# Kernel tuning notes

Hardware: AMD Instinct MI355X
Metric: run time of the kernel (lower is better)

The kernel has to match this reference:

```python
import jax, jax.numpy as jnp
import numpy as np

HEAD_NUM = 8
QKV_DIM = 16
SQRT_EMB = 11.313708498984761  # sqrt(128)
LOGIT_CLIP = 10.0
SOFTMAX_TEMP = 0.1


def _heads(x):
    # [B, n, H*d] -> [B, H, n, d]
    b, n, _ = x.shape
    return x.reshape(b, n, HEAD_NUM, QKV_DIM).transpose(0, 2, 1, 3)


def setup_inputs() -> dict:
    key = jax.random.key(0)
    ks = jax.random.split(key, 8)
    B, P, N, E = 32, 512, 1024, 128
    s = 1.0 / np.sqrt(E)
    return {
        "encoded_last_node": jax.random.normal(ks[0], (B, P, E), jnp.float32),
        "load": jax.random.uniform(ks[1], (B, P), jnp.float32),
        "ninf_mask": jnp.zeros((B, P, N), jnp.float32),
        "encoded_nodes": jax.random.normal(ks[2], (B, N, E), jnp.float32),
        "Wq_last": jax.random.normal(ks[3], (E + 1, E), jnp.float32) * s,
        "Wk": jax.random.normal(ks[4], (E, E), jnp.float32) * s,
        "Wv": jax.random.normal(ks[5], (E, E), jnp.float32) * s,
        "Wc": jax.random.normal(ks[6], (E, E), jnp.float32) * s,
        "bc": jnp.zeros((E,), jnp.float32),
    }


def reference(encoded_last_node, load, ninf_mask, encoded_nodes, Wq_last, Wk, Wv, Wc, bc):
    # set_kv
    k = _heads(encoded_nodes @ Wk)              # [B,H,N,d]
    v = _heads(encoded_nodes @ Wv)              # [B,H,N,d]

    # forward
    input_cat = jnp.concatenate([encoded_last_node, load[:, :, None]], axis=2)  # [B,P,E+1]
    q = _heads(input_cat @ Wq_last)             # [B,H,P,d]

    score = jnp.einsum("bhpd,bhnd->bhpn", q, k) / jnp.sqrt(jnp.float32(QKV_DIM))
    score = score + ninf_mask[:, None, :, :]
    weights = jax.nn.softmax(score, axis=3)
    out = jnp.einsum("bhpn,bhnd->bhpd", weights, v)
    out_concat = out.transpose(0, 2, 1, 3).reshape(q.shape[0], q.shape[2], HEAD_NUM * QKV_DIM)
    mh_atten_out = out_concat @ Wc + bc         # [B,P,E]

    # single-head tanh-clipped scoring against encoded_nodes
    s = jnp.einsum("bpe,bne->bpn", mh_atten_out, encoded_nodes) / SQRT_EMB
    s = LOGIT_CLIP * jnp.tanh(s) + ninf_mask
    probs = jax.nn.softmax(s / SOFTMAX_TEMP, axis=2)
    return probs
```

## Files before the change

kernel.cpp:

```cpp
#include <hip/hip_runtime.h>
#include <math.h>
#include <stdint.h>

#define B_ 32
#define P_ 512
#define N_ 1024
#define E_ 128
#define H_ 8
#define D_ 16

typedef unsigned short ushort_t;
typedef __attribute__((ext_vector_type(8))) short short8;
typedef __attribute__((ext_vector_type(4))) float f32x4;

union U8 { short8 s8; uint32_t u[4]; };

__device__ __forceinline__ void fma4(float4& acc, float a, float4 w) {
  acc.x = fmaf(a, w.x, acc.x); acc.y = fmaf(a, w.y, acc.y);
  acc.z = fmaf(a, w.z, acc.z); acc.w = fmaf(a, w.w, acc.w);
}
__device__ __forceinline__ void add4(float4& acc, float4 w) {
  acc.x += w.x; acc.y += w.y; acc.z += w.z; acc.w += w.w;
}
__device__ __forceinline__ float fast_tanh(float x) {
  x = fminf(20.f, fmaxf(-20.f, x));
  float e = __expf(2.f * x);
  return (e - 1.f) / (e + 1.f);
}
__device__ __forceinline__ uint32_t f32_to_hl(float x) {
  uint32_t bits = __float_as_uint(x);
  uint32_t hi = bits >> 16;
  float rem = x - __uint_as_float(bits & 0xFFFF0000u);
  uint32_t lo = __float_as_uint(rem) >> 16;
  return hi | (lo << 16);
}

__global__ __launch_bounds__(256, 2) void gemm128(
    const float* __restrict__ A, const float* __restrict__ W,
    const float* __restrict__ ea, const float* __restrict__ ew,
    const float* __restrict__ bias, float* __restrict__ C) {
  __shared__ float As[128][33];
  __shared__ float Ws[32][128];
  const int tid = threadIdx.x;
  const size_t m0 = (size_t)blockIdx.x * 128;
  const int tr = tid >> 3, tc = tid & 7;
  const int r0 = tr * 4;
  const int c0 = tc * 16;

  float4 acc[4][4];
#pragma unroll
  for (int j = 0; j < 4; ++j)
#pragma unroll
    for (int i = 0; i < 4; ++i) acc[j][i] = make_float4(0.f, 0.f, 0.f, 0.f);

  for (int kb = 0; kb < 4; ++kb) {
    __syncthreads();
    {
      int idx = tid;
#pragma unroll
      for (int it = 0; it < 4; ++it, idx += 256) {
        int r = idx >> 3, k4 = idx & 7;
        float4 v = reinterpret_cast<const float4*>(A + (m0 + r) * 128 + kb * 32)[k4];
        As[r][k4 * 4 + 0] = v.x; As[r][k4 * 4 + 1] = v.y;
        As[r][k4 * 4 + 2] = v.z; As[r][k4 * 4 + 3] = v.w;
      }
      idx = tid;
#pragma unroll
      for (int it = 0; it < 4; ++it, idx += 256) {
        int kk = idx >> 5, c4 = idx & 31;
        reinterpret_cast<float4*>(&Ws[kk][0])[c4] =
            reinterpret_cast<const float4*>(W + (size_t)(kb * 32 + kk) * 128)[c4];
      }
    }
    __syncthreads();
#pragma unroll 8
    for (int kk = 0; kk < 32; ++kk) {
      float a0 = As[r0 + 0][kk], a1 = As[r0 + 1][kk];
      float a2 = As[r0 + 2][kk], a3 = As[r0 + 3][kk];
      const float4* wr = reinterpret_cast<const float4*>(&Ws[kk][c0]);
      float4 w0 = wr[0], w1 = wr[1], w2 = wr[2], w3 = wr[3];
      fma4(acc[0][0], a0, w0); fma4(acc[0][1], a0, w1); fma4(acc[0][2], a0, w2); fma4(acc[0][3], a0, w3);
      fma4(acc[1][0], a1, w0); fma4(acc[1][1], a1, w1); fma4(acc[1][2], a1, w2); fma4(acc[1][3], a1, w3);
      fma4(acc[2][0], a2, w0); fma4(acc[2][1], a2, w1); fma4(acc[2][2], a2, w2); fma4(acc[2][3], a2, w3);
      fma4(acc[3][0], a3, w0); fma4(acc[3][1], a3, w1); fma4(acc[3][2], a3, w2); fma4(acc[3][3], a3, w3);
    }
  }

  if (ea != nullptr) {
    const float4* ew4 = reinterpret_cast<const float4*>(ew + c0);
    float4 e0 = ew4[0], e1 = ew4[1], e2 = ew4[2], e3 = ew4[3];
#pragma unroll
    for (int j = 0; j < 4; ++j) {
      float av = ea[m0 + r0 + j];
      fma4(acc[j][0], av, e0); fma4(acc[j][1], av, e1);
      fma4(acc[j][2], av, e2); fma4(acc[j][3], av, e3);
    }
  }
  if (bias != nullptr) {
    const float4* b4 = reinterpret_cast<const float4*>(bias + c0);
    float4 b0 = b4[0], b1 = b4[1], b2 = b4[2], b3 = b4[3];
#pragma unroll
    for (int j = 0; j < 4; ++j) {
      add4(acc[j][0], b0); add4(acc[j][1], b1); add4(acc[j][2], b2); add4(acc[j][3], b3);
    }
  }
#pragma unroll
  for (int j = 0; j < 4; ++j) {
    float4* c4p = reinterpret_cast<float4*>(C + (m0 + r0 + j) * 128 + c0);
    c4p[0] = acc[j][0]; c4p[1] = acc[j][1]; c4p[2] = acc[j][2]; c4p[3] = acc[j][3];
  }
}

__global__ __launch_bounds__(256, 1) void gemm_kv(
    const float* __restrict__ A, const float* __restrict__ Wk,
    const float* __restrict__ Wv, ushort_t* __restrict__ khl,
    ushort_t* __restrict__ vthl) {
  __shared__ float As[128][33];
  __shared__ float Wks[32][128];
  __shared__ float Wvs[32][128];
  const int tid = threadIdx.x;
  const size_t m0 = (size_t)blockIdx.x * 128;
  const int tr = tid >> 3, tc = tid & 7;
  const int r0 = tr * 4;
  const int c0 = tc * 16;

  float4 acck[4][4], accv[4][4];
#pragma unroll
  for (int j = 0; j < 4; ++j)
#pragma unroll
    for (int i = 0; i < 4; ++i) {
      acck[j][i] = make_float4(0.f, 0.f, 0.f, 0.f);
      accv[j][i] = make_float4(0.f, 0.f, 0.f, 0.f);
    }

  for (int kb = 0; kb < 4; ++kb) {
    __syncthreads();
    {
      int idx = tid;
#pragma unroll
      for (int it = 0; it < 4; ++it, idx += 256) {
        int r = idx >> 3, k4 = idx & 7;
        float4 v = reinterpret_cast<const float4*>(A + (m0 + r) * 128 + kb * 32)[k4];
        As[r][k4 * 4 + 0] = v.x; As[r][k4 * 4 + 1] = v.y;
        As[r][k4 * 4 + 2] = v.z; As[r][k4 * 4 + 3] = v.w;
      }
      idx = tid;
#pragma unroll
      for (int it = 0; it < 4; ++it, idx += 256) {
        int kk = idx >> 5, c4 = idx & 31;
        reinterpret_cast<float4*>(&Wks[kk][0])[c4] =
            reinterpret_cast<const float4*>(Wk + (size_t)(kb * 32 + kk) * 128)[c4];
      }
      idx = tid;
#pragma unroll
      for (int it = 0; it < 4; ++it, idx += 256) {
        int kk = idx >> 5, c4 = idx & 31;
        reinterpret_cast<float4*>(&Wvs[kk][0])[c4] =
            reinterpret_cast<const float4*>(Wv + (size_t)(kb * 32 + kk) * 128)[c4];
      }
    }
    __syncthreads();
#pragma unroll 4
    for (int kk = 0; kk < 32; ++kk) {
      float a0 = As[r0 + 0][kk], a1 = As[r0 + 1][kk];
      float a2 = As[r0 + 2][kk], a3 = As[r0 + 3][kk];
      const float4* wkr = reinterpret_cast<const float4*>(&Wks[kk][c0]);
      const float4* wvr = reinterpret_cast<const float4*>(&Wvs[kk][c0]);
#pragma unroll
      for (int i = 0; i < 4; ++i) {
        float4 wk = wkr[i], wv = wvr[i];
        fma4(acck[0][i], a0, wk); fma4(acck[1][i], a1, wk);
        fma4(acck[2][i], a2, wk); fma4(acck[3][i], a3, wk);
        fma4(accv[0][i], a0, wv); fma4(accv[1][i], a1, wv);
        fma4(accv[2][i], a2, wv); fma4(accv[3][i], a3, wv);
      }
    }
  }

#pragma unroll
  for (int j = 0; j < 4; ++j) {
    ushort_t* krow = khl + (m0 + r0 + j) * 256;
#pragma unroll
    for (int i = 0; i < 4; ++i) {
      uint4 pk;
      pk.x = f32_to_hl(acck[j][i].x);
      pk.y = f32_to_hl(acck[j][i].y);
      pk.z = f32_to_hl(acck[j][i].z);
      pk.w = f32_to_hl(acck[j][i].w);
      *reinterpret_cast<uint4*>(krow + 2 * (c0 + 4 * i)) = pk;
    }
  }
  const int bb = (int)(m0 >> 10);
  const int nbase = (int)(m0 & 1023) + r0;
#pragma unroll
  for (int i = 0; i < 4; ++i) {
#pragma unroll
    for (int e = 0; e < 4; ++e) {
      const int c = c0 + 4 * i + e;
      const int hh = c >> 4, dd = c & 15;
      uint4 pv;
      pv.x = f32_to_hl(reinterpret_cast<const float*>(&accv[0][i])[e]);
      pv.y = f32_to_hl(reinterpret_cast<const float*>(&accv[1][i])[e]);
      pv.z = f32_to_hl(reinterpret_cast<const float*>(&accv[2][i])[e]);
      pv.w = f32_to_hl(reinterpret_cast<const float*>(&accv[3][i])[e]);
      *reinterpret_cast<uint4*>(
          vthl + (size_t)((bb * H_ + hh) * 16 + dd) * 2048 + 2 * nbase) = pv;
    }
  }
}

__global__ __launch_bounds__(256, 2) void gemm_q(
    const float* __restrict__ A, const float* __restrict__ W,
    const float* __restrict__ ea, const float* __restrict__ ew,
    ushort_t* __restrict__ qhl) {
  __shared__ float As[128][33];
  __shared__ float Ws[32][128];
  const int tid = threadIdx.x;
  const size_t m0 = (size_t)blockIdx.x * 128;
  const int tr = tid >> 3, tc = tid & 7;
  const int r0 = tr * 4;
  const int c0 = tc * 16;

  float4 acc[4][4];
#pragma unroll
  for (int j = 0; j < 4; ++j)
#pragma unroll
    for (int i = 0; i < 4; ++i) acc[j][i] = make_float4(0.f, 0.f, 0.f, 0.f);

  for (int kb = 0; kb < 4; ++kb) {
    __syncthreads();
    {
      int idx = tid;
#pragma unroll
      for (int it = 0; it < 4; ++it, idx += 256) {
        int r = idx >> 3, k4 = idx & 7;
        float4 v = reinterpret_cast<const float4*>(A + (m0 + r) * 128 + kb * 32)[k4];
        As[r][k4 * 4 + 0] = v.x; As[r][k4 * 4 + 1] = v.y;
        As[r][k4 * 4 + 2] = v.z; As[r][k4 * 4 + 3] = v.w;
      }
      idx = tid;
#pragma unroll
      for (int it = 0; it < 4; ++it, idx += 256) {
        int kk = idx >> 5, c4 = idx & 31;
        reinterpret_cast<float4*>(&Ws[kk][0])[c4] =
            reinterpret_cast<const float4*>(W + (size_t)(kb * 32 + kk) * 128)[c4];
      }
    }
    __syncthreads();
#pragma unroll 8
    for (int kk = 0; kk < 32; ++kk) {
      float a0 = As[r0 + 0][kk], a1 = As[r0 + 1][kk];
      float a2 = As[r0 + 2][kk], a3 = As[r0 + 3][kk];
      const float4* wr = reinterpret_cast<const float4*>(&Ws[kk][c0]);
      float4 w0 = wr[0], w1 = wr[1], w2 = wr[2], w3 = wr[3];
      fma4(acc[0][0], a0, w0); fma4(acc[0][1], a0, w1); fma4(acc[0][2], a0, w2); fma4(acc[0][3], a0, w3);
      fma4(acc[1][0], a1, w0); fma4(acc[1][1], a1, w1); fma4(acc[1][2], a1, w2); fma4(acc[1][3], a1, w3);
      fma4(acc[2][0], a2, w0); fma4(acc[2][1], a2, w1); fma4(acc[2][2], a2, w2); fma4(acc[2][3], a2, w3);
      fma4(acc[3][0], a3, w0); fma4(acc[3][1], a3, w1); fma4(acc[3][2], a3, w2); fma4(acc[3][3], a3, w3);
    }
  }

  {
    const float4* ew4 = reinterpret_cast<const float4*>(ew + c0);
    float4 e0 = ew4[0], e1 = ew4[1], e2 = ew4[2], e3 = ew4[3];
#pragma unroll
    for (int j = 0; j < 4; ++j) {
      float av = ea[m0 + r0 + j];
      fma4(acc[j][0], av, e0); fma4(acc[j][1], av, e1);
      fma4(acc[j][2], av, e2); fma4(acc[j][3], av, e3);
    }
  }
#pragma unroll
  for (int j = 0; j < 4; ++j) {
    ushort_t* qrow = qhl + (m0 + r0 + j) * 256;
#pragma unroll
    for (int i = 0; i < 4; ++i) {
      uint4 pq;
      pq.x = f32_to_hl(acc[j][i].x);
      pq.y = f32_to_hl(acc[j][i].y);
      pq.z = f32_to_hl(acc[j][i].z);
      pq.w = f32_to_hl(acc[j][i].w);
      *reinterpret_cast<uint4*>(qrow + 2 * (c0 + 4 * i)) = pq;
    }
  }
}

__global__ __launch_bounds__(256, 4) void attn_mfma(
    const ushort_t* __restrict__ qhl, const ushort_t* __restrict__ khl,
    const ushort_t* __restrict__ vthl, const float* __restrict__ mask,
    float* __restrict__ O) {
  const int b = blockIdx.z, h = blockIdx.y, pt = blockIdx.x;
  const int tid = threadIdx.x;
  const int w = tid >> 6, lane = tid & 63;
  const int lp = lane & 15, g = lane >> 4;
  const int pA = pt * 128 + w * 16 + lp;
  const int pB = pA + 64;

  __shared__ __align__(16) ushort_t Ks[64 * 40];
  __shared__ __align__(16) ushort_t VTs[16 * 136];

  U8 qA1u, qA2u, qB1u, qB2u;
  {
    uint4 qldA = *reinterpret_cast<const uint4*>(
        qhl + (size_t)(b * P_ + pA) * 256 + h * 32 + g * 8);
    uint4 qldB = *reinterpret_cast<const uint4*>(
        qhl + (size_t)(b * P_ + pB) * 256 + h * 32 + g * 8);
    uint32_t a[4] = {qldA.x, qldA.y, qldA.z, qldA.w};
    uint32_t c[4] = {qldB.x, qldB.y, qldB.z, qldB.w};
#pragma unroll
    for (int i = 0; i < 4; ++i) {
      uint32_t lo16 = a[i] & 0xFFFFu;
      qA1u.u[i] = lo16 | (lo16 << 16);
      qA2u.u[i] = a[i] >> 16;
      uint32_t lo16b = c[i] & 0xFFFFu;
      qB1u.u[i] = lo16b | (lo16b << 16);
      qB2u.u[i] = c[i] >> 16;
    }
  }
  const short8 qA1 = qA1u.s8, qA2 = qA2u.s8, qB1 = qB1u.s8, qB2 = qB2u.s8;

  const float* mrowA = mask + (size_t)(b * P_ + pA) * N_;
  const float* mrowB = mask + (size_t)(b * P_ + pB) * N_;

  f32x4 accA = {0.f, 0.f, 0.f, 0.f}, accB = {0.f, 0.f, 0.f, 0.f};
  float mA = -1e30f, lA = 0.f, mB = -1e30f, lB = 0.f;

  for (int ch = 0; ch < N_ / 64; ++ch) {
    const int n0 = ch * 64;
    __syncthreads();
    {
      const int n = tid >> 2, seg = tid & 3;
      uint4 kv = *reinterpret_cast<const uint4*>(
          khl + (size_t)(b * N_ + n0 + n) * 256 + h * 32 + seg * 8);
      *reinterpret_cast<uint4*>(Ks + n * 40 + seg * 8) = kv;
      const int d = tid >> 4, s2 = tid & 15;
      uint4 vv = *reinterpret_cast<const uint4*>(
          vthl + (size_t)((b * H_ + h) * 16 + d) * 2048 + n0 * 2 + s2 * 8);
      *reinterpret_cast<uint4*>(VTs + d * 136 + s2 * 8) = vv;
    }
    __syncthreads();

    float svA[4][4], svB[4][4];
    float cmA = -1e30f, cmB = -1e30f;
#pragma unroll
    for (int tt = 0; tt < 4; ++tt) {
      short8 ka = *reinterpret_cast<const short8*>(Ks + (tt * 16 + lp) * 40 + g * 8);
      f32x4 aA = {0.f, 0.f, 0.f, 0.f};
      aA = __builtin_amdgcn_mfma_f32_16x16x32_bf16(ka, qA1, aA, 0, 0, 0);
      aA = __builtin_amdgcn_mfma_f32_16x16x32_bf16(ka, qA2, aA, 0, 0, 0);
      f32x4 aB = {0.f, 0.f, 0.f, 0.f};
      aB = __builtin_amdgcn_mfma_f32_16x16x32_bf16(ka, qB1, aB, 0, 0, 0);
      aB = __builtin_amdgcn_mfma_f32_16x16x32_bf16(ka, qB2, aB, 0, 0, 0);
      float4 mvA = *reinterpret_cast<const float4*>(mrowA + n0 + tt * 16 + g * 4);
      float4 mvB = *reinterpret_cast<const float4*>(mrowB + n0 + tt * 16 + g * 4);
      svA[tt][0] = fmaf(aA[0], 0.25f, mvA.x);
      svA[tt][1] = fmaf(aA[1], 0.25f, mvA.y);
      svA[tt][2] = fmaf(aA[2], 0.25f, mvA.z);
      svA[tt][3] = fmaf(aA[3], 0.25f, mvA.w);
      svB[tt][0] = fmaf(aB[0], 0.25f, mvB.x);
      svB[tt][1] = fmaf(aB[1], 0.25f, mvB.y);
      svB[tt][2] = fmaf(aB[2], 0.25f, mvB.z);
      svB[tt][3] = fmaf(aB[3], 0.25f, mvB.w);
      cmA = fmaxf(cmA, fmaxf(fmaxf(svA[tt][0], svA[tt][1]), fmaxf(svA[tt][2], svA[tt][3])));
      cmB = fmaxf(cmB, fmaxf(fmaxf(svB[tt][0], svB[tt][1]), fmaxf(svB[tt][2], svB[tt][3])));
    }
    cmA = fmaxf(cmA, __shfl_xor(cmA, 16));
    cmB = fmaxf(cmB, __shfl_xor(cmB, 16));
    cmA = fmaxf(cmA, __shfl_xor(cmA, 32));
    cmB = fmaxf(cmB, __shfl_xor(cmB, 32));
    const float nmA = fmaxf(mA, cmA), nmB = fmaxf(mB, cmB);
    const float fA = __expf(mA - nmA), fB = __expf(mB - nmB);
    accA[0] *= fA; accA[1] *= fA; accA[2] *= fA; accA[3] *= fA;
    accB[0] *= fB; accB[1] *= fB; accB[2] *= fB; accB[3] *= fB;
    float lsA = 0.f, lsB = 0.f;
#pragma unroll
    for (int tt = 0; tt < 4; ++tt)
#pragma unroll
      for (int r = 0; r < 4; ++r) {
        float eA = __expf(svA[tt][r] - nmA);
        float eB = __expf(svB[tt][r] - nmB);
        svA[tt][r] = eA; lsA += eA;
        svB[tt][r] = eB; lsB += eB;
      }
    lsA += __shfl_xor(lsA, 16); lsB += __shfl_xor(lsB, 16);
    lsA += __shfl_xor(lsA, 32); lsB += __shfl_xor(lsB, 32);
    lA = lA * fA + lsA; mA = nmA;
    lB = lB * fB + lsB; mB = nmB;

#pragma unroll
    for (int tt = 0; tt < 4; ++tt) {
      U8 pA1, pA2, pB1, pB2;
#pragma unroll
      for (int r = 0; r < 4; ++r) {
        uint32_t ba = __float_as_uint(svA[tt][r]);
        uint32_t ha = ba >> 16;
        float rema = svA[tt][r] - __uint_as_float(ba & 0xFFFF0000u);
        pA1.u[r] = ha | (ha << 16);
        pA2.u[r] = __float_as_uint(rema) >> 16;
        uint32_t bb2 = __float_as_uint(svB[tt][r]);
        uint32_t hb = bb2 >> 16;
        float remb = svB[tt][r] - __uint_as_float(bb2 & 0xFFFF0000u);
        pB1.u[r] = hb | (hb << 16);
        pB2.u[r] = __float_as_uint(remb) >> 16;
      }
      short8 va = *reinterpret_cast<const short8*>(VTs + lp * 136 + tt * 32 + g * 8);
      accA = __builtin_amdgcn_mfma_f32_16x16x32_bf16(va, pA1.s8, accA, 0, 0, 0);
      accA = __builtin_amdgcn_mfma_f32_16x16x32_bf16(va, pA2.s8, accA, 0, 0, 0);
      accB = __builtin_amdgcn_mfma_f32_16x16x32_bf16(va, pB1.s8, accB, 0, 0, 0);
      accB = __builtin_amdgcn_mfma_f32_16x16x32_bf16(va, pB2.s8, accB, 0, 0, 0);
    }
  }

  const float invA = 1.f / lA, invB = 1.f / lB;
  float4 oA, oB;
  oA.x = accA[0] * invA; oA.y = accA[1] * invA; oA.z = accA[2] * invA; oA.w = accA[3] * invA;
  oB.x = accB[0] * invB; oB.y = accB[1] * invB; oB.z = accB[2] * invB; oB.w = accB[3] * invB;
  *reinterpret_cast<float4*>(O + (size_t)(b * P_ + pA) * E_ + h * 16 + g * 4) = oA;
  *reinterpret_cast<float4*>(O + (size_t)(b * P_ + pB) * E_ + h * 16 + g * 4) = oB;
}

__global__ __launch_bounds__(256, 4) void logits_mfma(
    const float* __restrict__ mh, const float* __restrict__ enc,
    const float* __restrict__ mask, float* __restrict__ T) {
  const int b = blockIdx.z;
  const int p0 = blockIdx.y * 64;
  const int nq = blockIdx.x;
  const int tid = threadIdx.x;
  const int w = tid >> 6, lane = tid & 63;
  const int lp = lane & 15, g = lane >> 4;
  const int p = p0 + w * 16 + lp;

  __shared__ __align__(16) ushort_t Es[64 * 264];

  U8 fb1[8], fb2[8];
  {
    const float* mrow_mh = mh + (size_t)(b * P_ + p) * E_;
#pragma unroll
    for (int win = 0; win < 8; ++win) {
      float4 v = *reinterpret_cast<const float4*>(mrow_mh + win * 16 + g * 4);
      float vv[4] = {v.x, v.y, v.z, v.w};
#pragma unroll
      for (int r = 0; r < 4; ++r) {
        uint32_t bits = __float_as_uint(vv[r]);
        uint32_t hh = bits >> 16;
        float rem = vv[r] - __uint_as_float(bits & 0xFFFF0000u);
        fb1[win].u[r] = hh | (hh << 16);
        fb2[win].u[r] = __float_as_uint(rem) >> 16;
      }
    }
  }

  const float* mrow = mask + (size_t)(b * P_ + p) * N_ + nq * 256;
  float* trow = T + (size_t)(b * P_ + p) * N_ + nq * 256;
  const float inv_s = 0.08838834764831845f;

  for (int ch = 0; ch < 4; ++ch) {
    const int n0g = nq * 256 + ch * 64;
    __syncthreads();
    {
      int idx = tid;
#pragma unroll
      for (int it = 0; it < 8; ++it, idx += 256) {
        const int r = idx >> 5, f4 = idx & 31;
        float4 v = *reinterpret_cast<const float4*>(
            enc + ((size_t)b * N_ + n0g + r) * E_ + f4 * 4);
        uint4 o;
        o.x = f32_to_hl(v.x); o.y = f32_to_hl(v.y);
        o.z = f32_to_hl(v.z); o.w = f32_to_hl(v.w);
        *reinterpret_cast<uint4*>(Es + r * 264 + f4 * 8) = o;
      }
    }
    __syncthreads();

#pragma unroll
    for (int tt = 0; tt < 4; ++tt) {
      f32x4 acc = {0.f, 0.f, 0.f, 0.f};
#pragma unroll
      for (int win = 0; win < 8; ++win) {
        short8 ea = *reinterpret_cast<const short8*>(
            Es + (tt * 16 + lp) * 264 + win * 32 + g * 8);
        acc = __builtin_amdgcn_mfma_f32_16x16x32_bf16(ea, fb1[win].s8, acc, 0, 0, 0);
        acc = __builtin_amdgcn_mfma_f32_16x16x32_bf16(ea, fb2[win].s8, acc, 0, 0, 0);
      }
      float4 mv = *reinterpret_cast<const float4*>(mrow + ch * 64 + tt * 16 + g * 4);
      float4 o;
      o.x = fmaf(10.f, fast_tanh(acc[0] * inv_s), mv.x);
      o.y = fmaf(10.f, fast_tanh(acc[1] * inv_s), mv.y);
      o.z = fmaf(10.f, fast_tanh(acc[2] * inv_s), mv.z);
      o.w = fmaf(10.f, fast_tanh(acc[3] * inv_s), mv.w);
      *reinterpret_cast<float4*>(trow + ch * 64 + tt * 16 + g * 4) = o;
    }
  }
}

__global__ __launch_bounds__(256, 4) void softmax_rows(
    const float* __restrict__ T, float* __restrict__ O) {
  const size_t row = blockIdx.x;
  const int tid = threadIdx.x;
  const float4 v = reinterpret_cast<const float4*>(T + row * N_)[tid];
  float lm = fmaxf(fmaxf(v.x, v.y), fmaxf(v.z, v.w));
#pragma unroll
  for (int o = 32; o; o >>= 1) lm = fmaxf(lm, __shfl_xor(lm, o));
  __shared__ float red[8];
  const int wave = tid >> 6, lane = tid & 63;
  if (lane == 0) red[wave] = lm;
  __syncthreads();
  const float m = fmaxf(fmaxf(red[0], red[1]), fmaxf(red[2], red[3]));
  float4 w;
  w.x = __expf((v.x - m) * 10.f);
  w.y = __expf((v.y - m) * 10.f);
  w.z = __expf((v.z - m) * 10.f);
  w.w = __expf((v.w - m) * 10.f);
  float ls = w.x + w.y + w.z + w.w;
#pragma unroll
  for (int o = 32; o; o >>= 1) ls += __shfl_xor(ls, o);
  if (lane == 0) red[4 + wave] = ls;
  __syncthreads();
  const float inv = 1.f / (red[4] + red[5] + red[6] + red[7]);
  float4 o4;
  o4.x = w.x * inv; o4.y = w.y * inv; o4.z = w.z * inv; o4.w = w.w * inv;
  reinterpret_cast<float4*>(O + row * N_)[tid] = o4;
}

extern "C" void kernel_launch(void* const* d_in, const int* in_sizes, int n_in,
                              void* d_out, int out_size, void* d_ws, size_t ws_size,
                              hipStream_t stream) {
  const float* eln  = (const float*)d_in[0];
  const float* load = (const float*)d_in[1];
  const float* mask = (const float*)d_in[2];
  const float* enc  = (const float*)d_in[3];
  const float* Wq   = (const float*)d_in[4];
  const float* Wk   = (const float*)d_in[5];
  const float* Wv   = (const float*)d_in[6];
  const float* Wc   = (const float*)d_in[7];
  const float* bc   = (const float*)d_in[8];
  float* out = (float*)d_out;

  char* base = (char*)d_ws;
  ushort_t* khl  = (ushort_t*)base;
  ushort_t* vthl = (ushort_t*)(base + 16777216);
  ushort_t* qhl  = (ushort_t*)(base + 2 * 16777216);
  float* mhbuf   = (float*)(base + 2 * 16777216);
  float* tbuf    = (float*)(base + 2 * 16777216 + 8388608);
  float* abuf    = tbuf;

  gemm_kv<<<dim3(256), 256, 0, stream>>>(enc, Wk, Wv, khl, vthl);
  gemm_q<<<dim3(128), 256, 0, stream>>>(eln, Wq, load, Wq + 128 * 128, qhl);
  attn_mfma<<<dim3(P_ / 128, H_, B_), 256, 0, stream>>>(qhl, khl, vthl, mask, abuf);
  gemm128<<<dim3(128), 256, 0, stream>>>(abuf, Wc, nullptr, nullptr, bc, mhbuf);
  logits_mfma<<<dim3(4, 8, B_), 256, 0, stream>>>(mhbuf, enc, mask, tbuf);
  softmax_rows<<<dim3(16384), 256, 0, stream>>>(tbuf, out);
}
```

Before: 357.6 us.

## Split attention over key halves with combine pass; shrink GEMM tiles for more blocks

Attention now splits the key dimension into two halves per block (split-K flash-decoding style), writing partial outputs plus max/sum, and a new combine kernel merges them with rescaling. The projection GEMMs use smaller row tiles (64 for KV, 32 for Q and output projection) to launch more blocks and raise occupancy. This doubles attention grid parallelism at the cost of an extra kernel launch and extra partial-result traffic through global memory.

Result: slower. 544.2 us (+52.2%).

```diff
diff --git a/kernel.cpp b/kernel.cpp
--- a/kernel.cpp
+++ b/kernel.cpp
@@ -8,6 +8,7 @@
 #define E_ 128
 #define H_ 8
 #define D_ 16
+#define BHP_ (B_ * H_ * P_)
 
 typedef unsigned short ushort_t;
 typedef __attribute__((ext_vector_type(8))) short short8;
@@ -18,9 +19,6 @@
 __device__ __forceinline__ void fma4(float4& acc, float a, float4 w) {
   acc.x = fmaf(a, w.x, acc.x); acc.y = fmaf(a, w.y, acc.y);
   acc.z = fmaf(a, w.z, acc.z); acc.w = fmaf(a, w.w, acc.w);
-}
-__device__ __forceinline__ void add4(float4& acc, float4 w) {
-  acc.x += w.x; acc.y += w.y; acc.z += w.z; acc.w += w.w;
 }
 __device__ __forceinline__ float fast_tanh(float x) {
   x = fminf(20.f, fmaxf(-20.f, x));
@@ -35,30 +33,34 @@
   return hi | (lo << 16);
 }
 
-__global__ __launch_bounds__(256, 2) void gemm128(
-    const float* __restrict__ A, const float* __restrict__ W,
-    const float* __restrict__ ea, const float* __restrict__ ew,
-    const float* __restrict__ bias, float* __restrict__ C) {
-  __shared__ float As[128][33];
-  __shared__ float Ws[32][128];
+__global__ __launch_bounds__(256, 3) void gemm_kv(
+    const float* __restrict__ A, const float* __restrict__ Wk,
+    const float* __restrict__ Wv, ushort_t* __restrict__ khl,
+    ushort_t* __restrict__ vthl) {
+  __shared__ float As[64][33];
+  __shared__ float Wks[32][128];
+  __shared__ float Wvs[32][128];
   const int tid = threadIdx.x;
-  const size_t m0 = (size_t)blockIdx.x * 128;
+  const size_t m0 = (size_t)blockIdx.x * 64;
   const int tr = tid >> 3, tc = tid & 7;
-  const int r0 = tr * 4;
+  const int r0 = tr * 2;
   const int c0 = tc * 16;
 
-  float4 acc[4][4];
-#pragma unroll
-  for (int j = 0; j < 4; ++j)
-#pragma unroll
-    for (int i = 0; i < 4; ++i) acc[j][i] = make_float4(0.f, 0.f, 0.f, 0.f);
+  float4 acck[2][4], accv[2][4];
+#pragma unroll
+  for (int j = 0; j < 2; ++j)
+#pragma unroll
+    for (int i = 0; i < 4; ++i) {
+      acck[j][i] = make_float4(0.f, 0.f, 0.f, 0.f);
+      accv[j][i] = make_float4(0.f, 0.f, 0.f, 0.f);
+    }
 
   for (int kb = 0; kb < 4; ++kb) {
     __syncthreads();
     {
       int idx = tid;
 #pragma unroll
-      for (int it = 0; it < 4; ++it, idx += 256) {
+      for (int it = 0; it < 2; ++it, idx += 256) {
         int r = idx >> 3, k4 = idx & 7;
         float4 v = reinterpret_cast<const float4*>(A + (m0 + r) * 128 + kb * 32)[k4];
         As[r][k4 * 4 + 0] = v.x; As[r][k4 * 4 + 1] = v.y;
@@ -68,86 +70,6 @@
 #pragma unroll
       for (int it = 0; it < 4; ++it, idx += 256) {
         int kk = idx >> 5, c4 = idx & 31;
-        reinterpret_cast<float4*>(&Ws[kk][0])[c4] =
-            reinterpret_cast<const float4*>(W + (size_t)(kb * 32 + kk) * 128)[c4];
-      }
-    }
-    __syncthreads();
-#pragma unroll 8
-    for (int kk = 0; kk < 32; ++kk) {
-      float a0 = As[r0 + 0][kk], a1 = As[r0 + 1][kk];
-      float a2 = As[r0 + 2][kk], a3 = As[r0 + 3][kk];
-      const float4* wr = reinterpret_cast<const float4*>(&Ws[kk][c0]);
-      float4 w0 = wr[0], w1 = wr[1], w2 = wr[2], w3 = wr[3];
-      fma4(acc[0][0], a0, w0); fma4(acc[0][1], a0, w1); fma4(acc[0][2], a0, w2); fma4(acc[0][3], a0, w3);
-      fma4(acc[1][0], a1, w0); fma4(acc[1][1], a1, w1); fma4(acc[1][2], a1, w2); fma4(acc[1][3], a1, w3);
-      fma4(acc[2][0], a2, w0); fma4(acc[2][1], a2, w1); fma4(acc[2][2], a2, w2); fma4(acc[2][3], a2, w3);
-      fma4(acc[3][0], a3, w0); fma4(acc[3][1], a3, w1); fma4(acc[3][2], a3, w2); fma4(acc[3][3], a3, w3);
-    }
-  }
-
-  if (ea != nullptr) {
-    const float4* ew4 = reinterpret_cast<const float4*>(ew + c0);
-    float4 e0 = ew4[0], e1 = ew4[1], e2 = ew4[2], e3 = ew4[3];
-#pragma unroll
-    for (int j = 0; j < 4; ++j) {
-      float av = ea[m0 + r0 + j];
-      fma4(acc[j][0], av, e0); fma4(acc[j][1], av, e1);
-      fma4(acc[j][2], av, e2); fma4(acc[j][3], av, e3);
-    }
-  }
-  if (bias != nullptr) {
-    const float4* b4 = reinterpret_cast<const float4*>(bias + c0);
-    float4 b0 = b4[0], b1 = b4[1], b2 = b4[2], b3 = b4[3];
-#pragma unroll
-    for (int j = 0; j < 4; ++j) {
-      add4(acc[j][0], b0); add4(acc[j][1], b1); add4(acc[j][2], b2); add4(acc[j][3], b3);
-    }
-  }
-#pragma unroll
-  for (int j = 0; j < 4; ++j) {
-    float4* c4p = reinterpret_cast<float4*>(C + (m0 + r0 + j) * 128 + c0);
-    c4p[0] = acc[j][0]; c4p[1] = acc[j][1]; c4p[2] = acc[j][2]; c4p[3] = acc[j][3];
-  }
-}
-
-__global__ __launch_bounds__(256, 1) void gemm_kv(
-    const float* __restrict__ A, const float* __restrict__ Wk,
-    const float* __restrict__ Wv, ushort_t* __restrict__ khl,
-    ushort_t* __restrict__ vthl) {
-  __shared__ float As[128][33];
-  __shared__ float Wks[32][128];
-  __shared__ float Wvs[32][128];
-  const int tid = threadIdx.x;
-  const size_t m0 = (size_t)blockIdx.x * 128;
-  const int tr = tid >> 3, tc = tid & 7;
-  const int r0 = tr * 4;
-  const int c0 = tc * 16;
-
-  float4 acck[4][4], accv[4][4];
-#pragma unroll
-  for (int j = 0; j < 4; ++j)
-#pragma unroll
-    for (int i = 0; i < 4; ++i) {
-      acck[j][i] = make_float4(0.f, 0.f, 0.f, 0.f);
-      accv[j][i] = make_float4(0.f, 0.f, 0.f, 0.f);
-    }
-
-  for (int kb = 0; kb < 4; ++kb) {
-    __syncthreads();
-    {
-      int idx = tid;
-#pragma unroll
-      for (int it = 0; it < 4; ++it, idx += 256) {
-        int r = idx >> 3, k4 = idx & 7;
-        float4 v = reinterpret_cast<const float4*>(A + (m0 + r) * 128 + kb * 32)[k4];
-        As[r][k4 * 4 + 0] = v.x; As[r][k4 * 4 + 1] = v.y;
-        As[r][k4 * 4 + 2] = v.z; As[r][k4 * 4 + 3] = v.w;
-      }
-      idx = tid;
-#pragma unroll
-      for (int it = 0; it < 4; ++it, idx += 256) {
-        int kk = idx >> 5, c4 = idx & 31;
         reinterpret_cast<float4*>(&Wks[kk][0])[c4] =
             reinterpret_cast<const float4*>(Wk + (size_t)(kb * 32 + kk) * 128)[c4];
       }
@@ -160,25 +82,22 @@
       }
     }
     __syncthreads();
-#pragma unroll 4
+#pragma unroll 8
     for (int kk = 0; kk < 32; ++kk) {
       float a0 = As[r0 + 0][kk], a1 = As[r0 + 1][kk];
-      float a2 = As[r0 + 2][kk], a3 = As[r0 + 3][kk];
       const float4* wkr = reinterpret_cast<const float4*>(&Wks[kk][c0]);
       const float4* wvr = reinterpret_cast<const float4*>(&Wvs[kk][c0]);
 #pragma unroll
       for (int i = 0; i < 4; ++i) {
         float4 wk = wkr[i], wv = wvr[i];
         fma4(acck[0][i], a0, wk); fma4(acck[1][i], a1, wk);
-        fma4(acck[2][i], a2, wk); fma4(acck[3][i], a3, wk);
         fma4(accv[0][i], a0, wv); fma4(accv[1][i], a1, wv);
-        fma4(accv[2][i], a2, wv); fma4(accv[3][i], a3, wv);
-      }
-    }
-  }
-
-#pragma unroll
-  for (int j = 0; j < 4; ++j) {
+      }
+    }
+  }
+
+#pragma unroll
+  for (int j = 0; j < 2; ++j) {
     ushort_t* krow = khl + (m0 + r0 + j) * 256;
 #pragma unroll
     for (int i = 0; i < 4; ++i) {
@@ -198,47 +117,38 @@
     for (int e = 0; e < 4; ++e) {
       const int c = c0 + 4 * i + e;
       const int hh = c >> 4, dd = c & 15;
-      uint4 pv;
+      uint2 pv;
       pv.x = f32_to_hl(reinterpret_cast<const float*>(&accv[0][i])[e]);
       pv.y = f32_to_hl(reinterpret_cast<const float*>(&accv[1][i])[e]);
-      pv.z = f32_to_hl(reinterpret_cast<const float*>(&accv[2][i])[e]);
-      pv.w = f32_to_hl(reinterpret_cast<const float*>(&accv[3][i])[e]);
-      *reinterpret_cast<uint4*>(
+      *reinterpret_cast<uint2*>(
           vthl + (size_t)((bb * H_ + hh) * 16 + dd) * 2048 + 2 * nbase) = pv;
     }
   }
 }
 
-__global__ __launch_bounds__(256, 2) void gemm_q(
+__global__ __launch_bounds__(256, 4) void gemm_q32(
     const float* __restrict__ A, const float* __restrict__ W,
     const float* __restrict__ ea, const float* __restrict__ ew,
     ushort_t* __restrict__ qhl) {
-  __shared__ float As[128][33];
+  __shared__ float As[32][33];
   __shared__ float Ws[32][128];
   const int tid = threadIdx.x;
-  const size_t m0 = (size_t)blockIdx.x * 128;
-  const int tr = tid >> 3, tc = tid & 7;
-  const int r0 = tr * 4;
-  const int c0 = tc * 16;
-
-  float4 acc[4][4];
-#pragma unroll
-  for (int j = 0; j < 4; ++j)
-#pragma unroll
-    for (int i = 0; i < 4; ++i) acc[j][i] = make_float4(0.f, 0.f, 0.f, 0.f);
+  const size_t m0 = (size_t)blockIdx.x * 32;
+  const int r0 = tid >> 3;
+  const int c0 = (tid & 7) * 16;
+
+  float4 acc[4];
+#pragma unroll
+  for (int i = 0; i < 4; ++i) acc[i] = make_float4(0.f, 0.f, 0.f, 0.f);
 
   for (int kb = 0; kb < 4; ++kb) {
     __syncthreads();
     {
+      int r = tid >> 3, k4 = tid & 7;
+      float4 v = reinterpret_cast<const float4*>(A + (m0 + r) * 128 + kb * 32)[k4];
+      As[r][k4 * 4 + 0] = v.x; As[r][k4 * 4 + 1] = v.y;
+      As[r][k4 * 4 + 2] = v.z; As[r][k4 * 4 + 3] = v.w;
       int idx = tid;
-#pragma unroll
-      for (int it = 0; it < 4; ++it, idx += 256) {
-        int r = idx >> 3, k4 = idx & 7;
-        float4 v = reinterpret_cast<const float4*>(A + (m0 + r) * 128 + kb * 32)[k4];
-        As[r][k4 * 4 + 0] = v.x; As[r][k4 * 4 + 1] = v.y;
-        As[r][k4 * 4 + 2] = v.z; As[r][k4 * 4 + 3] = v.w;
-      }
-      idx = tid;
 #pragma unroll
       for (int it = 0; it < 4; ++it, idx += 256) {
         int kk = idx >> 5, c4 = idx & 31;
@@ -249,47 +159,84 @@
     __syncthreads();
 #pragma unroll 8
     for (int kk = 0; kk < 32; ++kk) {
-      float a0 = As[r0 + 0][kk], a1 = As[r0 + 1][kk];
-      float a2 = As[r0 + 2][kk], a3 = As[r0 + 3][kk];
+      float a0 = As[r0][kk];
       const float4* wr = reinterpret_cast<const float4*>(&Ws[kk][c0]);
-      float4 w0 = wr[0], w1 = wr[1], w2 = wr[2], w3 = wr[3];
-      fma4(acc[0][0], a0, w0); fma4(acc[0][1], a0, w1); fma4(acc[0][2], a0, w2); fma4(acc[0][3], a0, w3);
-      fma4(acc[1][0], a1, w0); fma4(acc[1][1], a1, w1); fma4(acc[1][2], a1, w2); fma4(acc[1][3], a1, w3);
-      fma4(acc[2][0], a2, w0); fma4(acc[2][1], a2, w1); fma4(acc[2][2], a2, w2); fma4(acc[2][3], a2, w3);
-      fma4(acc[3][0], a3, w0); fma4(acc[3][1], a3, w1); fma4(acc[3][2], a3, w2); fma4(acc[3][3], a3, w3);
-    }
-  }
-
+      fma4(acc[0], a0, wr[0]); fma4(acc[1], a0, wr[1]);
+      fma4(acc[2], a0, wr[2]); fma4(acc[3], a0, wr[3]);
+    }
+  }
   {
     const float4* ew4 = reinterpret_cast<const float4*>(ew + c0);
-    float4 e0 = ew4[0], e1 = ew4[1], e2 = ew4[2], e3 = ew4[3];
-#pragma unroll
-    for (int j = 0; j < 4; ++j) {
-      float av = ea[m0 + r0 + j];
-      fma4(acc[j][0], av, e0); fma4(acc[j][1], av, e1);
-      fma4(acc[j][2], av, e2); fma4(acc[j][3], av, e3);
-    }
-  }
-#pragma unroll
-  for (int j = 0; j < 4; ++j) {
-    ushort_t* qrow = qhl + (m0 + r0 + j) * 256;
-#pragma unroll
-    for (int i = 0; i < 4; ++i) {
-      uint4 pq;
-      pq.x = f32_to_hl(acc[j][i].x);
-      pq.y = f32_to_hl(acc[j][i].y);
-      pq.z = f32_to_hl(acc[j][i].z);
-      pq.w = f32_to_hl(acc[j][i].w);
-      *reinterpret_cast<uint4*>(qrow + 2 * (c0 + 4 * i)) = pq;
-    }
-  }
-}
-
-__global__ __launch_bounds__(256, 4) void attn_mfma(
+    float av = ea[m0 + r0];
+    fma4(acc[0], av, ew4[0]); fma4(acc[1], av, ew4[1]);
+    fma4(acc[2], av, ew4[2]); fma4(acc[3], av, ew4[3]);
+  }
+  ushort_t* qrow = qhl + (m0 + r0) * 256;
+#pragma unroll
+  for (int i = 0; i < 4; ++i) {
+    uint4 pq;
+    pq.x = f32_to_hl(acc[i].x); pq.y = f32_to_hl(acc[i].y);
+    pq.z = f32_to_hl(acc[i].z); pq.w = f32_to_hl(acc[i].w);
+    *reinterpret_cast<uint4*>(qrow + 2 * (c0 + 4 * i)) = pq;
+  }
+}
+
+__global__ __launch_bounds__(256, 4) void gemm_c32(
+    const float* __restrict__ A, const float* __restrict__ W,
+    const float* __restrict__ bias, float* __restrict__ C) {
+  __shared__ float As[32][33];
+  __shared__ float Ws[32][128];
+  const int tid = threadIdx.x;
+  const size_t m0 = (size_t)blockIdx.x * 32;
+  const int r0 = tid >> 3;
+  const int c0 = (tid & 7) * 16;
+
+  float4 acc[4];
+#pragma unroll
+  for (int i = 0; i < 4; ++i) acc[i] = make_float4(0.f, 0.f, 0.f, 0.f);
+
+  for (int kb = 0; kb < 4; ++kb) {
+    __syncthreads();
+    {
+      int r = tid >> 3, k4 = tid & 7;
+      float4 v = reinterpret_cast<const float4*>(A + (m0 + r) * 128 + kb * 32)[k4];
+      As[r][k4 * 4 + 0] = v.x; As[r][k4 * 4 + 1] = v.y;
+      As[r][k4 * 4 + 2] = v.z; As[r][k4 * 4 + 3] = v.w;
+      int idx = tid;
+#pragma unroll
+      for (int it = 0; it < 4; ++it, idx += 256) {
+        int kk = idx >> 5, c4 = idx & 31;
+        reinterpret_cast<float4*>(&Ws[kk][0])[c4] =
+            reinterpret_cast<const float4*>(W + (size_t)(kb * 32 + kk) * 128)[c4];
+      }
+    }
+    __syncthreads();
+#pragma unroll 8
+    for (int kk = 0; kk < 32; ++kk) {
+      float a0 = As[r0][kk];
+      const float4* wr = reinterpret_cast<const float4*>(&Ws[kk][c0]);
+      fma4(acc[0], a0, wr[0]); fma4(acc[1], a0, wr[1]);
+      fma4(acc[2], a0, wr[2]); fma4(acc[3], a0, wr[3]);
+    }
+  }
+  const float4* b4 = reinterpret_cast<const float4*>(bias + c0);
+  float4* c4p = reinterpret_cast<float4*>(C + (m0 + r0) * 128 + c0);
+#pragma unroll
+  for (int i = 0; i < 4; ++i) {
+    float4 bv = b4[i];
+    float4 o = acc[i];
+    o.x += bv.x; o.y += bv.y; o.z += bv.z; o.w += bv.w;
+    c4p[i] = o;
+  }
+}
+
+__global__ __launch_bounds__(256, 8) void attn_pass(
     const ushort_t* __restrict__ qhl, const ushort_t* __restrict__ khl,
     const ushort_t* __restrict__ vthl, const float* __restrict__ mask,
-    float* __restrict__ O) {
-  const int b = blockIdx.z, h = blockIdx.y, pt = blockIdx.x;
+    float* __restrict__ pout, float* __restrict__ pml) {
+  const int b = blockIdx.z, h = blockIdx.y;
+  const int pt = blockIdx.x >> 1;
+  const int ns = blockIdx.x & 1;
   const int tid = threadIdx.x;
   const int w = tid >> 6, lane = tid & 63;
   const int lp = lane & 15, g = lane >> 4;
@@ -325,8 +272,8 @@
   f32x4 accA = {0.f, 0.f, 0.f, 0.f}, accB = {0.f, 0.f, 0.f, 0.f};
   float mA = -1e30f, lA = 0.f, mB = -1e30f, lB = 0.f;
 
-  for (int ch = 0; ch < N_ / 64; ++ch) {
-    const int n0 = ch * 64;
+  for (int ch = 0; ch < 8; ++ch) {
+    const int n0 = ns * 512 + ch * 64;
     __syncthreads();
     {
       const int n = tid >> 2, seg = tid & 3;
@@ -411,12 +358,44 @@
     }
   }
 
-  const float invA = 1.f / lA, invB = 1.f / lB;
+  const size_t idxA = (size_t)(b * H_ + h) * P_ + pA;
+  const size_t idxB = (size_t)(b * H_ + h) * P_ + pB;
   float4 oA, oB;
-  oA.x = accA[0] * invA; oA.y = accA[1] * invA; oA.z = accA[2] * invA; oA.w = accA[3] * invA;
-  oB.x = accB[0] * invB; oB.y = accB[1] * invB; oB.z = accB[2] * invB; oB.w = accB[3] * invB;
-  *reinterpret_cast<float4*>(O + (size_t)(b * P_ + pA) * E_ + h * 16 + g * 4) = oA;
-  *reinterpret_cast<float4*>(O + (size_t)(b * P_ + pB) * E_ + h * 16 + g * 4) = oB;
+  oA.x = accA[0]; oA.y = accA[1]; oA.z = accA[2]; oA.w = accA[3];
+  oB.x = accB[0]; oB.y = accB[1]; oB.z = accB[2]; oB.w = accB[3];
+  *reinterpret_cast<float4*>(pout + ((size_t)ns * BHP_ + idxA) * 16 + g * 4) = oA;
+  *reinterpret_cast<float4*>(pout + ((size_t)ns * BHP_ + idxB) * 16 + g * 4) = oB;
+  if (g == 0) {
+    reinterpret_cast<float2*>(pml)[(size_t)ns * BHP_ + idxA] = make_float2(mA, lA);
+    reinterpret_cast<float2*>(pml)[(size_t)ns * BHP_ + idxB] = make_float2(mB, lB);
+  }
+}
+
+__global__ __launch_bounds__(256, 8) void attn_combine(
+    const float* __restrict__ pout, const float* __restrict__ pml,
+    float* __restrict__ O) {
+  const int idx = blockIdx.x * 256 + threadIdx.x;
+  const int b = idx >> 12;
+  const int h = (idx >> 9) & 7;
+  const int p = idx & 511;
+  float2 ml0 = reinterpret_cast<const float2*>(pml)[idx];
+  float2 ml1 = reinterpret_cast<const float2*>(pml)[BHP_ + idx];
+  const float M = fmaxf(ml0.x, ml1.x);
+  const float w0 = __expf(ml0.x - M), w1 = __expf(ml1.x - M);
+  const float inv = 1.f / (ml0.y * w0 + ml1.y * w1);
+  const float4* p0 = reinterpret_cast<const float4*>(pout + (size_t)idx * 16);
+  const float4* p1 = reinterpret_cast<const float4*>(pout + ((size_t)BHP_ + idx) * 16);
+  float4* o4 = reinterpret_cast<float4*>(O + (size_t)(b * P_ + p) * E_ + h * 16);
+#pragma unroll
+  for (int i = 0; i < 4; ++i) {
+    float4 a = p0[i], c = p1[i];
+    float4 o;
+    o.x = (a.x * w0 + c.x * w1) * inv;
+    o.y = (a.y * w0 + c.y * w1) * inv;
+    o.z = (a.z * w0 + c.z * w1) * inv;
+    o.w = (a.w * w0 + c.w * w1) * inv;
+    o4[i] = o;
+  }
 }
 
 __global__ __launch_bounds__(256, 4) void logits_mfma(
@@ -543,11 +522,14 @@
   float* mhbuf   = (float*)(base + 2 * 16777216);
   float* tbuf    = (float*)(base + 2 * 16777216 + 8388608);
   float* abuf    = tbuf;
-
-  gemm_kv<<<dim3(256), 256, 0, stream>>>(enc, Wk, Wv, khl, vthl);
-  gemm_q<<<dim3(128), 256, 0, stream>>>(eln, Wq, load, Wq + 128 * 128, qhl);
-  attn_mfma<<<dim3(P_ / 128, H_, B_), 256, 0, stream>>>(qhl, khl, vthl, mask, abuf);
-  gemm128<<<dim3(128), 256, 0, stream>>>(abuf, Wc, nullptr, nullptr, bc, mhbuf);
+  float* pout    = (float*)((char*)tbuf + 8388608);
+  float* pml     = (float*)((char*)tbuf + 8388608 + 16777216);
+
+  gemm_kv<<<dim3(512), 256, 0, stream>>>(enc, Wk, Wv, khl, vthl);
+  gemm_q32<<<dim3(512), 256, 0, stream>>>(eln, Wq, load, Wq + 128 * 128, qhl);
+  attn_pass<<<dim3(8, H_, B_), 256, 0, stream>>>(qhl, khl, vthl, mask, pout, pml);
+  attn_combine<<<dim3(BHP_ / 256), 256, 0, stream>>>(pout, pml, abuf);
+  gemm_c32<<<dim3(512), 256, 0, stream>>>(abuf, Wc, bc, mhbuf);
   logits_mfma<<<dim3(4, 8, B_), 256, 0, stream>>>(mhbuf, enc, mask, tbuf);
   softmax_rows<<<dim3(16384), 256, 0, stream>>>(tbuf, out);
 }
```
